# Kernel tuning notes

Hardware: AMD Instinct MI355X
Metric: run time of the kernel (lower is better)

## Reference

```python
import jax, jax.numpy as jnp
import numpy as np

B, T, C, H, K = 2, 1024, 2048, 32, 64
D_MIX, D_DEC, FF = 32, 64, 7168
GN_EPS = 1e-5 * 8 ** 2  # GroupNorm eps = 1e-5 * head_size_divisor**2


def setup_inputs() -> dict:
    key = jax.random.key(0)
    ks = jax.random.split(key, 40)
    nrm = lambda i, sh, s=0.02: jax.random.normal(ks[i], sh, jnp.float32) * s
    uni = lambda i, sh: jax.random.uniform(ks[i], sh, jnp.float32)
    return {
        'x': jax.random.normal(ks[0], (B, T, C), jnp.float32),
        'time_mix_shift': jax.random.normal(ks[1], (B, 1, C), jnp.float32),
        'channel_mix_state': jax.random.normal(ks[2], (B, 1, C), jnp.float32),
        'time_mix_state': jax.random.normal(ks[3], (B, H, K, K), jnp.float32) * 0.1,
        'ln1_w': jnp.ones((C,), jnp.float32), 'ln1_b': jnp.zeros((C,), jnp.float32),
        'ln2_w': jnp.ones((C,), jnp.float32), 'ln2_b': jnp.zeros((C,), jnp.float32),
        'maa_x': uni(4, (1, 1, C)), 'maa_w': uni(5, (1, 1, C)), 'maa_k': uni(6, (1, 1, C)),
        'maa_v': uni(7, (1, 1, C)), 'maa_r': uni(8, (1, 1, C)), 'maa_g': uni(9, (1, 1, C)),
        'maa_w1': nrm(10, (C, 5 * D_MIX), 0.01), 'maa_w2': nrm(11, (5, D_MIX, C), 0.01),
        'td': jnp.linspace(-6.0, -1.0, C, dtype=jnp.float32).reshape(1, 1, C),
        'td_w1': nrm(12, (C, D_DEC), 0.01), 'td_w2': nrm(13, (D_DEC, C), 0.01),
        'u': nrm(14, (H, K), 0.05),
        'Wr': nrm(15, (C, C)), 'Wk': nrm(16, (C, C)), 'Wv': nrm(17, (C, C)),
        'Wg': nrm(18, (C, C)), 'Wo': nrm(19, (C, C)),
        'lnx_w': jnp.ones((C,), jnp.float32), 'lnx_b': jnp.zeros((C,), jnp.float32),
        'fmaa_k': uni(20, (1, 1, C)), 'fmaa_r': uni(21, (1, 1, C)),
        'fWk': nrm(22, (FF, C)), 'fWr': nrm(23, (C, C)), 'fWv': nrm(24, (C, FF)),
    }


def _ln(x, w, b, eps=1e-5):
    m = x.mean(-1, keepdims=True)
    v = jnp.var(x, axis=-1, keepdims=True)
    return (x - m) * jax.lax.rsqrt(v + eps) * w + b


def reference(x, time_mix_shift, channel_mix_state, time_mix_state,
              ln1_w, ln1_b, ln2_w, ln2_b,
              maa_x, maa_w, maa_k, maa_v, maa_r, maa_g, maa_w1, maa_w2,
              td, td_w1, td_w2, u, Wr, Wk, Wv, Wg, Wo, lnx_w, lnx_b,
              fmaa_k, fmaa_r, fWk, fWr, fWv):
    # ---- TimeMix (att) on ln1(x) ----
    xn = _ln(x, ln1_w, ln1_b)
    prev = jnp.concatenate([time_mix_shift, xn[:, :-1]], axis=1)  # [B,T,C]
    new_shift = xn[:, -1:]
    xx = prev - xn
    hh = jnp.tanh((xn + xx * maa_x) @ maa_w1).reshape(B, T, 5, D_MIX)
    mm = jnp.einsum('btfd,fdc->fbtc', hh, maa_w2)
    xw = xn + xx * (maa_w + mm[0])
    xk = xn + xx * (maa_k + mm[1])
    xv = xn + xx * (maa_v + mm[2])
    xr = xn + xx * (maa_r + mm[3])
    xg = xn + xx * (maa_g + mm[4])
    r = xr @ Wr.T
    k = xk @ Wk.T
    v = xv @ Wv.T
    g = jax.nn.silu(xg @ Wg.T)
    # log-decay w = -exp(time_decay + LoRA(xw)); per-step decay factor is exp(w)
    w = -jnp.exp(td + jnp.tanh(xw @ td_w1) @ td_w2)
    # WKV6 recurrence over T (state [B,H,K,K])
    rs, ks_, vs, ws = (jnp.moveaxis(a.reshape(B, T, H, K), 1, 0) for a in (r, k, v, w))

    def step(s, inp):
        r_t, k_t, v_t, w_t = inp  # each [B,H,K]
        kv = jnp.einsum('bhk,bhv->bhkv', k_t, v_t)
        o_t = jnp.einsum('bhk,bhkv->bhv', r_t, s + u[None, :, :, None] * kv)
        s = jnp.exp(w_t)[..., None] * s + kv
        return s, o_t

    new_wkv, o = jax.lax.scan(step, time_mix_state, (rs, ks_, vs, ws))
    o = jnp.moveaxis(o, 0, 1)  # [B,T,H,K]
    # GroupNorm over heads (groups=H, channels=K each)
    mu = o.mean(-1, keepdims=True)
    var = jnp.var(o, axis=-1, keepdims=True)
    y = ((o - mu) * jax.lax.rsqrt(var + GN_EPS)).reshape(B, T, C) * lnx_w + lnx_b
    x = x + (y * g) @ Wo.T
    # ---- ChannelMix (ffn) on ln2(x) ----
    xn2 = _ln(x, ln2_w, ln2_b)
    prev2 = jnp.concatenate([channel_mix_state, xn2[:, :-1]], axis=1)
    new_cm = xn2[:, -1:]
    xk2 = prev2 * fmaa_k + xn2 * (1.0 - fmaa_k)
    xr2 = prev2 * fmaa_r + xn2 * (1.0 - fmaa_r)
    kv2 = (jax.nn.relu(xk2 @ fWk.T) ** 2) @ fWv.T
    x = x + jax.nn.sigmoid(xr2 @ fWr.T) * kv2
    return (x, new_shift, new_cm, new_wkv)
```

## Files before the change

### kernel.cpp

```cpp
#include <hip/hip_runtime.h>
#include <hip/hip_bf16.h>
#include <math.h>

#define BB 2
#define TT 1024
#define CC 2048
#define HH 32
#define KK 64
#define BTROWS (BB*TT)
#define FFD 7168
#define LCH 64
#define NCH (TT/LCH)

typedef unsigned short ushort_t;
typedef __bf16 bf16x8 __attribute__((ext_vector_type(8)));
typedef float f32x4 __attribute__((ext_vector_type(4)));

__device__ __forceinline__ ushort_t f2bf(float f) {
  unsigned int u = __float_as_uint(f);
  u += 0x7fff + ((u >> 16) & 1);
  return (ushort_t)(u >> 16);
}

__device__ __forceinline__ void gload16(const ushort_t* g, ushort_t* l) {
// ... 192 lines not shown
      *(float4*)&bb[4] = *(const float4*)&Bs[k][tx * 8 + 4];
#pragma unroll
      for (int i = 0; i < 8; ++i)
#pragma unroll
        for (int j = 0; j < 8; ++j) acc[i][j] = fmaf(a[i], bb[j], acc[i][j]);
    }
    __syncthreads();
  }
#pragma unroll
  for (int i = 0; i < 8; ++i) {
    int row = m0 + ty * 8 + i;
#pragma unroll
    for (int j = 0; j < 8; ++j) {
      int col = n0 + tx * 8 + j;
      out[(size_t)row * N + col] = -expf(td[col] + acc[i][j]);
    }
  }
}

struct Mix5Args {
  const float* maa[5];
  float* xw;
  ushort_t* ob[4];
};

__global__ __launch_bounds__(256) void mix5_gemm(
    const float* __restrict__ hh, const float* __restrict__ w2,
    const float* __restrict__ xn, const float* __restrict__ tms, Mix5Args args) {
  const int f = blockIdx.y;
  const int rb = blockIdx.x;
  const int tid = threadIdx.x;
  __shared__ float hh8[8][32];
  {
    int r = tid >> 5, k = tid & 31;
    hh8[r][k] = hh[(size_t)(rb * 8 + r) * 160 + f * 32 + k];
  }
  __syncthreads();
  const float* maa = args.maa[f];
  const float* w2f = w2 + (size_t)f * 32 * CC;
#pragma unroll
  for (int chunk = 0; chunk < 2; ++chunk) {
    const int col = chunk * 1024 + tid * 4;
    float4 w2v[32];
#pragma unroll
    for (int k = 0; k < 32; ++k)
      w2v[k] = *(const float4*)(w2f + (size_t)k * CC + col);
    const float4 maa4 = *(const float4*)(maa + col);
#pragma unroll
    for (int r = 0; r < 8; ++r) {
      const int row = rb * 8 + r;
      float4 acc = {0.f, 0.f, 0.f, 0.f};
#pragma unroll
      for (int k4 = 0; k4 < 8; ++k4) {
        float4 h = *(const float4*)&hh8[r][k4 * 4];
        FMA4(acc, h.x, w2v[k4 * 4 + 0]);
        FMA4(acc, h.y, w2v[k4 * 4 + 1]);
        FMA4(acc, h.z, w2v[k4 * 4 + 2]);
        FMA4(acc, h.w, w2v[k4 * 4 + 3]);
      }
      const int t = row & (TT - 1);
      const size_t oi = (size_t)row * CC + col;
      float4 xv = *(const float4*)(xn + oi);
      float4 pv;
      if (t == 0) pv = *(const float4*)(tms + (size_t)(row >> 10) * CC + col);
      else        pv = *(const float4*)(xn + oi - CC);
      float4 v;
      v.x = xv.x + (pv.x - xv.x) * (maa4.x + acc.x);
      v.y = xv.y + (pv.y - xv.y) * (maa4.y + acc.y);
      v.z = xv.z + (pv.z - xv.z) * (maa4.z + acc.z);
      v.w = xv.w + (pv.w - xv.w) * (maa4.w + acc.w);
      if (f == 0) {
        *(float4*)(args.xw + oi) = v;
      } else {
        ushort4 o;
        o.x = f2bf(v.x); o.y = f2bf(v.y); o.z = f2bf(v.z); o.w = f2bf(v.w);
        *(ushort4*)(args.ob[f - 1] + oi) = o;
      }
    }
  }
}


template <bool IS_A>
__device__ __forceinline__ void g9_stage(
    char* buf, const ushort_t* g, int ld, int r0, int k0, int tid) {
  constexpr int NJ = IS_A ? 4 : 2;
  char* dst = buf + (IS_A ? 0 : 32768);
#pragma unroll
  for (int j = 0; j < NJ; ++j) {
    int L = j * 8192 + tid * 16;
    int P = L ^ (((L >> 7) & 7) << 4);
    int r = P >> 7, cb = (P & 127) >> 1;
    gload16(g + (size_t)(r0 + r) * ld + k0 + cb, (ushort_t*)(dst + L));
  }
}

__device__ __forceinline__ void g9_core(
    const ushort_t* gA, int lda, const ushort_t* gB, int ldb,
    int m0, int n0, int kstart, int K, char* lds, f32x4 (*acc)[4]) {
  const int tid = threadIdx.x, w = tid >> 6, l = tid & 63;
  const int wr = w >> 1, wc = w & 1;
  const int r16 = l & 15, h16 = (l >> 4) * 16;
  const int NT = K >> 6;
  g9_stage<true>(lds, gA, lda, m0, kstart, tid);
  g9_stage<false>(lds, gB, ldb, n0, kstart, tid);
  g9_stage<true>(lds + 49152, gA, lda, m0, kstart + 64, tid);
  g9_stage<false>(lds + 49152, gB, ldb, n0, kstart + 64, tid);
  int cur = 0;
  for (int t = 0; t < NT; ++t) {
    char* bufc = lds + cur * 49152;
    int nxt = cur + 2; if (nxt >= 3) nxt -= 3;
    char* bufn = lds + nxt * 49152;
    if (t + 1 < NT) asm volatile("s_waitcnt vmcnt(6)" ::: "memory");
    else            asm volatile("s_waitcnt vmcnt(0)" ::: "memory");
    __builtin_amdgcn_s_barrier();
    const bool pf = (t + 2 < NT);
    const int k2 = kstart + (t + 2) * 64;
    {
      bf16x8 a[4], b[4];
#pragma unroll
      for (int mf = 0; mf < 4; ++mf) {
        int row = wr * 64 + mf * 16 + r16;
        int off = h16 ^ ((row & 7) << 4);
        a[mf] = *(const bf16x8*)(bufc + row * 128 + off);
      }
#pragma unroll
      for (int nf = 0; nf < 4; ++nf) {
        int row = wc * 64 + nf * 16 + r16;
        int off = h16 ^ ((row & 7) << 4);
        b[nf] = *(const bf16x8*)(bufc + 32768 + row * 128 + off);
      }
      if (pf) g9_stage<true>(bufn, gA, lda, m0, k2, tid);
      __builtin_amdgcn_s_setprio(1);
#pragma unroll
      for (int mf = 0; mf < 4; ++mf)
#pragma unroll
        for (int nf = 0; nf < 4; ++nf)
          acc[mf][nf] = __builtin_amdgcn_mfma_f32_16x16x32_bf16(a[mf], b[nf], acc[mf][nf], 0, 0, 0);
      __builtin_amdgcn_s_setprio(0);
    }
    {
      bf16x8 a[4], b[4];
#pragma unroll
      for (int mf = 0; mf < 4; ++mf) {
        int row = wr * 64 + mf * 16 + r16;
        int off = (64 + h16) ^ ((row & 7) << 4);
        a[mf] = *(const bf16x8*)(bufc + row * 128 + off);
      }
#pragma unroll
      for (int nf = 0; nf < 4; ++nf) {
        int row = wc * 64 + nf * 16 + r16;
        int off = (64 + h16) ^ ((row & 7) << 4);
        b[nf] = *(const bf16x8*)(bufc + 32768 + row * 128 + off);
      }
      if (pf) g9_stage<false>(bufn, gB, ldb, n0, k2, tid);
      __builtin_amdgcn_s_setprio(1);
#pragma unroll
      for (int mf = 0; mf < 4; ++mf)
#pragma unroll
        for (int nf = 0; nf < 4; ++nf)
          acc[mf][nf] = __builtin_amdgcn_mfma_f32_16x16x32_bf16(a[mf], b[nf], acc[mf][nf], 0, 0, 0);
      __builtin_amdgcn_s_setprio(0);
    }
    cur += 1; if (cur == 3) cur = 0;
  }
}

#define G9_INIT_ACC f32x4 acc[4][4]; \
  _Pragma("unroll") for (int i0 = 0; i0 < 4; ++i0) \
  _Pragma("unroll") for (int i1 = 0; i1 < 4; ++i1) acc[i0][i1] = {0.f, 0.f, 0.f, 0.f};

struct RkvgArgs {
  const ushort_t* A[4];
  const ushort_t* W[4];
  float* O[4];
};

__global__ __launch_bounds__(512, 2) void g9_rkvg(RkvgArgs args) {
  __shared__ __align__(16) char lds[147456];
  const int z = blockIdx.z;
  const int m0 = blockIdx.y * 256, n0 = blockIdx.x * 128;
  G9_INIT_ACC
  g9_core(args.A[z], CC, args.W[z], CC, m0, n0, 0, CC, lds, acc);
  const int tid = threadIdx.x, w = tid >> 6, l = tid & 63;
  const int wr = w >> 1, wc = w & 1, r16 = l & 15, q4 = (l >> 4) * 4;
  float* out = args.O[z];
  const bool silu = (z == 3);
#pragma unroll
  for (int mf = 0; mf < 4; ++mf)
#pragma unroll
    for (int nf = 0; nf < 4; ++nf) {
      int col = n0 + wc * 64 + nf * 16 + r16;
#pragma unroll
      for (int j = 0; j < 4; ++j) {
        int row = m0 + wr * 64 + mf * 16 + q4 + j;
        float v = acc[mf][nf][j];
        if (silu) v = v / (1.f + expf(-v));
        out[(size_t)row * CC + col] = v;
      }
    }
}

__global__ __launch_bounds__(512, 2) void g9_relu2(
    const ushort_t* __restrict__ A, int lda,
    const ushort_t* __restrict__ W, int ldb,
    ushort_t* __restrict__ out, int N, int K) {
  __shared__ __align__(16) char lds[147456];
  const int m0 = blockIdx.y * 256, n0 = blockIdx.x * 128;
  G9_INIT_ACC
  g9_core(A, lda, W, ldb, m0, n0, 0, K, lds, acc);
  const int tid = threadIdx.x, w = tid >> 6, l = tid & 63;
  const int wr = w >> 1, wc = w & 1, r16 = l & 15, q4 = (l >> 4) * 4;
#pragma unroll
  for (int mf = 0; mf < 4; ++mf)
#pragma unroll
    for (int nf = 0; nf < 4; ++nf) {
      int col = n0 + wc * 64 + nf * 16 + r16;
#pragma unroll
      for (int j = 0; j < 4; ++j) {
        int row = m0 + wr * 64 + mf * 16 + q4 + j;
        float r_ = fmaxf(acc[mf][nf][j], 0.f);
        out[(size_t)row * N + col] = f2bf(r_ * r_);
      }
    }
}

struct SkArgs {
  const ushort_t* A;
  const ushort_t* W;
  float* P[4];
  int lda, ldb, klen;
};

__global__ __launch_bounds__(512, 2) void g9_sk(SkArgs args) {
  __shared__ __align__(16) char lds[147456];
  const int z = blockIdx.z;
  const int m0 = blockIdx.y * 256, n0 = blockIdx.x * 128;
  G9_INIT_ACC
  g9_core(args.A, args.lda, args.W, args.ldb, m0, n0, z * args.klen, args.klen, lds, acc);
  const int tid = threadIdx.x, w = tid >> 6, l = tid & 63;
  const int wr = w >> 1, wc = w & 1, r16 = l & 15, q4 = (l >> 4) * 4;
  float* out = args.P[z];
#pragma unroll
  for (int mf = 0; mf < 4; ++mf)
#pragma unroll
    for (int nf = 0; nf < 4; ++nf) {
      int col = n0 + wc * 64 + nf * 16 + r16;
#pragma unroll
      for (int j = 0; j < 4; ++j) {
        int row = m0 + wr * 64 + mf * 16 + q4 + j;
        out[(size_t)row * CC + col] = acc[mf][nf][j];
      }
    }
}

__global__ __launch_bounds__(256) void comb_add4(
    const float* __restrict__ p0, const float* __restrict__ p1,
    const float* __restrict__ p2, const float* __restrict__ p3,
    const float* __restrict__ base, float* __restrict__ out, int n4) {
  int i = blockIdx.x * 256 + threadIdx.x;
  int stride = gridDim.x * 256;
  for (; i < n4; i += stride) {
    float4 a = ((const float4*)p0)[i];
    float4 b = ((const float4*)p1)[i];
    float4 c = ((const float4*)p2)[i];
    float4 d = ((const float4*)p3)[i];
    float4 e = ((const float4*)base)[i];
    float4 o = {e.x + a.x + b.x + c.x + d.x, e.y + a.y + b.y + c.y + d.y,
                e.z + a.z + b.z + c.z + d.z, e.w + a.w + b.w + c.w + d.w};
    ((float4*)out)[i] = o;
  }
}

__global__ __launch_bounds__(256) void comb_sig4(
    const float* __restrict__ p0, const float* __restrict__ p1,
    const float* __restrict__ p2, const float* __restrict__ p3,
    float* __restrict__ out, int n4) {
  int i = blockIdx.x * 256 + threadIdx.x;
  int stride = gridDim.x * 256;
  for (; i < n4; i += stride) {
    float4 a = ((const float4*)p0)[i];
    float4 b = ((const float4*)p1)[i];
    float4 c = ((const float4*)p2)[i];
    float4 d = ((const float4*)p3)[i];
    float4 o;
    o.x = 1.f / (1.f + expf(-(a.x + b.x + c.x + d.x)));
    o.y = 1.f / (1.f + expf(-(a.y + b.y + c.y + d.y)));
    o.z = 1.f / (1.f + expf(-(a.z + b.z + c.z + d.z)));
    o.w = 1.f / (1.f + expf(-(a.w + b.w + c.w + d.w)));
    ((float4*)out)[i] = o;
  }
}

__global__ __launch_bounds__(256) void comb_fma4(
    const float* __restrict__ p0, const float* __restrict__ p1,
    const float* __restrict__ p2, const float* __restrict__ p3,
    const float* __restrict__ x2, const float* __restrict__ sig,
    float* __restrict__ out, int n4) {
  int i = blockIdx.x * 256 + threadIdx.x;
  int stride = gridDim.x * 256;
  for (; i < n4; i += stride) {
    float4 a = ((const float4*)p0)[i];
    float4 b = ((const float4*)p1)[i];
    float4 c = ((const float4*)p2)[i];
    float4 d = ((const float4*)p3)[i];
    float4 xx = ((const float4*)x2)[i];
    float4 ss = ((const float4*)sig)[i];
    float4 o;
    o.x = fmaf(ss.x, a.x + b.x + c.x + d.x, xx.x);
    o.y = fmaf(ss.y, a.y + b.y + c.y + d.y, xx.y);
    o.z = fmaf(ss.z, a.z + b.z + c.z + d.z, xx.z);
    o.w = fmaf(ss.w, a.w + b.w + c.w + d.w, xx.w);
    ((float4*)out)[i] = o;
  }
}

__global__ __launch_bounds__(256) void wkv_chunk1(
    const float* __restrict__ r, const float* __restrict__ k,
    const float* __restrict__ v, const float* __restrict__ w,
    const float* __restrict__ u,
    float* __restrict__ rtG, float* __restrict__ Pg,
    float* __restrict__ dg, float* __restrict__ o_intra) {
  __shared__ __align__(16) float lds[4 * 4160];
  float* Ech = lds;
  float* Ach = lds;
  float* rtl = lds + 4160;
  float* ktl = lds + 2 * 4160;
  float* Vl  = lds + 3 * 4160;
  __shared__ float Dl[64], dl[64];
  const int c = blockIdx.x, bh = blockIdx.y;
  const int b = bh >> 5, h = bh & 31;
  const int tid = threadIdx.x;
  const size_t base = (size_t)b * TT * CC + (size_t)(c * LCH) * CC + h * KK;
  for (int i = 0; i < 16; ++i) {
    int e = tid + 256 * i;
    int row = e >> 6, col = e & 63;
    size_t g = base + (size_t)row * CC + col;
    rtl[row * 65 + col] = r[g];
    ktl[row * 65 + col] = k[g];
    Vl[row * 65 + col] = v[g];
  }
  if (tid < 64) {
    float cum = 0.f;
#pragma unroll 8
    for (int i = 0; i < 64; ++i) {
      cum += w[base + (size_t)i * CC + tid];
      Ech[i * 64 + tid] = cum;
    }
    float dd = expf(cum);
    dl[tid] = dd;
    dg[(size_t)(bh * NCH + c) * 64 + tid] = dd;
  }
  __syncthreads();
  {
    const int g = tid >> 6, kk = tid & 63;
    const float uk = u[h * KK + kk];
    for (int i = 0; i < 16; ++i) {
      int t = i * 4 + g;
      float Cv = Ech[t * 64 + kk];
      float Ev = (t == 0) ? 0.f : Ech[(t - 1) * 64 + kk];
      float rraw = rtl[t * 65 + kk];
      float kraw = ktl[t * 65 + kk];
      float rtv = rraw * expf(Ev);
      float ktv = kraw * expf(-Cv);
      rtl[t * 65 + kk] = rtv;
      ktl[t * 65 + kk] = ktv;
      rtG[((size_t)(bh * NCH + c) * 64 + t) * 64 + kk] = rtv;
      float prod = rraw * uk * kraw;
#pragma unroll
      for (int off = 32; off; off >>= 1) prod += __shfl_xor(prod, off);
      if (kk == 0) Dl[t] = prod;
    }
  }
  __syncthreads();
  {
    const int ti = tid >> 4, tj = tid & 15;
    float a4[4][4];
#pragma unroll
    for (int a = 0; a < 4; ++a)
#pragma unroll
      for (int q = 0; q < 4; ++q) a4[a][q] = 0.f;
    for (int kk = 0; kk < 64; ++kk) {
      float ra[4], kb[4];
#pragma unroll
      for (int a = 0; a < 4; ++a) ra[a] = rtl[(4 * ti + a) * 65 + kk];
#pragma unroll
      for (int q = 0; q < 4; ++q) kb[q] = ktl[(4 * tj + q) * 65 + kk];
#pragma unroll
      for (int a = 0; a < 4; ++a)
#pragma unroll
        for (int q = 0; q < 4; ++q) a4[a][q] = fmaf(ra[a], kb[q], a4[a][q]);
    }
#pragma unroll
    for (int a = 0; a < 4; ++a) {
      int i = 4 * ti + a;
// ... 141 lines not shown
    int row = e >> 6, col = e & 63;
    float val = (ol[row * 65 + col] - mul[row]) * rsl[row];
    val = val * lnw[h * KK + col] + lnb[h * KK + col];
    size_t gi = base + (size_t)row * CC + col;
    ym[gi] = f2bf(val * g[gi]);
  }
}

extern "C" void kernel_launch(void* const* d_in, const int* in_sizes, int n_in,
                              void* d_out, int out_size, void* d_ws, size_t ws_size,
                              hipStream_t stream) {
  const float* x    = (const float*)d_in[0];
  const float* tms  = (const float*)d_in[1];
  const float* cms  = (const float*)d_in[2];
  const float* tmstate = (const float*)d_in[3];
  const float* ln1_w = (const float*)d_in[4];
  const float* ln1_b = (const float*)d_in[5];
  const float* ln2_w = (const float*)d_in[6];
  const float* ln2_b = (const float*)d_in[7];
  const float* maa_x = (const float*)d_in[8];
  const float* maa_w = (const float*)d_in[9];
  const float* maa_k = (const float*)d_in[10];
  const float* maa_v = (const float*)d_in[11];
  const float* maa_r = (const float*)d_in[12];
  const float* maa_g = (const float*)d_in[13];
  const float* maa_w1 = (const float*)d_in[14];
  const float* maa_w2 = (const float*)d_in[15];
  const float* td    = (const float*)d_in[16];
  const float* td_w1 = (const float*)d_in[17];
  const float* td_w2 = (const float*)d_in[18];
  const float* u     = (const float*)d_in[19];
  const float* Wr    = (const float*)d_in[20];
  const float* Wk    = (const float*)d_in[21];
  const float* Wv    = (const float*)d_in[22];
  const float* Wg    = (const float*)d_in[23];
  const float* Wo    = (const float*)d_in[24];
  const float* lnx_w = (const float*)d_in[25];
  const float* lnx_b = (const float*)d_in[26];
  const float* fmk   = (const float*)d_in[27];
  const float* fmr   = (const float*)d_in[28];
  const float* fWk   = (const float*)d_in[29];
  const float* fWr   = (const float*)d_in[30];
  const float* fWv   = (const float*)d_in[31];
  (void)in_sizes; (void)n_in; (void)out_size;

  const size_t SLOT = (size_t)BTROWS * CC;
  float* F[7];
  for (int i = 0; i < 7; ++i) F[i] = (float*)d_ws + i * SLOT;
  ushort_t* B0 = (ushort_t*)((float*)d_ws + 7 * SLOT);
  ushort_t* B1 = B0 + SLOT;
  ushort_t* B2 = B1 + SLOT;
  ushort_t* B3 = B2 + SLOT;
  ushort_t* WBIG = B3 + SLOT;
  ushort_t* WrB = WBIG;
  ushort_t* WkB = WrB + (size_t)CC * CC;
  ushort_t* WvB = WkB + (size_t)CC * CC;
  ushort_t* WgB = WvB + (size_t)CC * CC;
  ushort_t* WoB = WBIG + (size_t)4 * CC * CC;
  ushort_t* fWvB = WoB + (size_t)CC * CC;
  float* hh  = (float*)(fWvB + (size_t)CC * FFD);
  float* tmpd = hh + (size_t)BTROWS * 160;
  size_t need = (size_t)((char*)(tmpd + (size_t)BTROWS * 64) - (char*)d_ws);
  if (ws_size < need) return;
  ushort_t* fWkB = WBIG;
  ushort_t* fWrB = WoB;
  ushort_t* h1   = (ushort_t*)F[5];

  float* rtG = F[1];
  float* o_intra = F[0];
  float* s_starts = (float*)B0;
  float* Pg = (float*)B2;
  float* dbuf = (float*)(WBIG + (size_t)FFD * CC);
  ushort_t* ym = B3;

  float* partsW1 = F[4];
  float* partsTD = F[5];

  float* out_x    = (float*)d_out;
  float* out_shift = out_x + (size_t)BB * TT * CC;
  float* out_cm   = out_shift + (size_t)BB * CC;
  float* out_wkv  = out_cm + (size_t)BB * CC;

  const dim3 blk256(256);
  const dim3 blk512(512);

  cvt_kernel<<<2048, blk256, 0, stream>>>(Wr, WrB, CC * CC / 4);
  cvt_kernel<<<2048, blk256, 0, stream>>>(Wk, WkB, CC * CC / 4);
  cvt_kernel<<<2048, blk256, 0, stream>>>(Wv, WvB, CC * CC / 4);
  cvt_kernel<<<2048, blk256, 0, stream>>>(Wg, WgB, CC * CC / 4);
  cvt_kernel<<<2048, blk256, 0, stream>>>(Wo, WoB, CC * CC / 4);
  cvt_kernel<<<2048, blk256, 0, stream>>>(fWv, fWvB, CC * FFD / 4);

  ln_kernel<<<BTROWS, blk256, 0, stream>>>(x, ln1_w, ln1_b, F[0], out_shift);
  mixin_kernel<<<(BTROWS * CC) / 256, blk256, 0, stream>>>(F[0], tms, maa_x, F[3]);
  gemm_splitk<<<dim3(BTROWS / 64, 3, 8), blk256, 0, stream>>>(
      F[3], CC, maa_w1, 160, partsW1, 3, CC / 8, BTROWS);
  combine_tanh<<<(BTROWS * 160 + 255) / 256, blk256, 0, stream>>>(
      partsW1, 192, BTROWS, 160, 8, hh);
  {
    Mix5Args ma;
    ma.maa[0] = maa_w; ma.maa[1] = maa_k; ma.maa[2] = maa_v; ma.maa[3] = maa_r; ma.maa[4] = maa_g;
    ma.xw = F[1];
    ma.ob[0] = B1; ma.ob[1] = B2; ma.ob[2] = B3; ma.ob[3] = B0;
    mix5_gemm<<<dim3(BTROWS / 8, 5), blk256, 0, stream>>>(hh, maa_w2, F[0], tms, ma);
  }
  gemm_splitk<<<dim3(BTROWS / 64, 1, 8), blk256, 0, stream>>>(
      F[1], CC, td_w1, 64, partsTD, 1, CC / 8, BTROWS);
  combine_tanh<<<(BTROWS * 64 + 255) / 256, blk256, 0, stream>>>(
      partsTD, 64, BTROWS, 64, 8, tmpd);
  gemm_negexp<<<dim3(16, 16), blk256, 0, stream>>>(tmpd, 64, td_w2, CC, F[2], CC, 64, td);
  {
    RkvgArgs ra;
    ra.A[0] = B3; ra.A[1] = B1; ra.A[2] = B2; ra.A[3] = B0;
    ra.W[0] = WrB; ra.W[1] = WkB; ra.W[2] = WvB; ra.W[3] = WgB;
    ra.O[0] = F[3]; ra.O[1] = F[4]; ra.O[2] = F[5]; ra.O[3] = F[6];
    g9_rkvg<<<dim3(16, 8, 4), blk512, 0, stream>>>(ra);
  }
  cvt_kernel<<<2048, blk256, 0, stream>>>(fWk, fWkB, FFD * CC / 4);
  wkv_chunk1<<<dim3(NCH, BB * HH), blk256, 0, stream>>>(
      F[3], F[4], F[5], F[2], u, rtG, Pg, dbuf, o_intra);
  wkv_chain<<<BB * HH, blk256, 0, stream>>>(Pg, dbuf, tmstate, s_starts, out_wkv);
  wkv_chunk2<<<dim3(NCH, BB * HH), blk256, 0, stream>>>(
      rtG, s_starts, o_intra, F[6], lnx_w, lnx_b, ym);
  {
    SkArgs sa;
    sa.A = ym; sa.W = WoB; sa.lda = CC; sa.ldb = CC; sa.klen = CC / 4;
    sa.P[0] = F[0]; sa.P[1] = F[1]; sa.P[2] = F[3]; sa.P[3] = F[4];
    g9_sk<<<dim3(16, 8, 4), blk512, 0, stream>>>(sa);
  }
  comb_add4<<<2048, blk256, 0, stream>>>(F[0], F[1], F[3], F[4], x, F[2], (int)(SLOT / 4));
  cvt_kernel<<<2048, blk256, 0, stream>>>(fWr, fWrB, CC * CC / 4);
  ln_kernel<<<BTROWS, blk256, 0, stream>>>(F[2], ln2_w, ln2_b, F[1], out_cm);
  mix2_kernel<<<(BTROWS * CC) / 256, blk256, 0, stream>>>(F[1], cms, fmk, fmr, B1, B2);
  g9_relu2<<<dim3(FFD / 128, 8), blk512, 0, stream>>>(B1, CC, fWkB, CC, h1, FFD, CC);
  {
    SkArgs ss;
    ss.A = B2; ss.W = fWrB; ss.lda = CC; ss.ldb = CC; ss.klen = CC / 4;
    ss.P[0] = F[0]; ss.P[1] = F[1]; ss.P[2] = F[3]; ss.P[3] = (float*)B3;
    g9_sk<<<dim3(16, 8, 4), blk512, 0, stream>>>(ss);
  }
  comb_sig4<<<2048, blk256, 0, stream>>>(F[0], F[1], F[3], (float*)B3, F[4], (int)(SLOT / 4));
  {
    SkArgs sf;
    sf.A = h1; sf.W = fWvB; sf.lda = FFD; sf.ldb = FFD; sf.klen = FFD / 4;
    sf.P[0] = F[0]; sf.P[1] = F[1]; sf.P[2] = F[3]; sf.P[3] = (float*)B0;
    g9_sk<<<dim3(16, 8, 4), blk512, 0, stream>>>(sf);
  }
  comb_fma4<<<2048, blk256, 0, stream>>>(
      F[0], F[1], F[3], (float*)B0, F[2], F[4], out_x, (int)(SLOT / 4));
}
```

Baseline: 726.0 us.

## Use 4-wave GEMM blocks with 128x64 per-wave tiles and 2-way split-K

The bf16 MFMA GEMM core now runs 256 threads per block instead of 512. The block tile stays 256x128, but each wave computes a 128x64 sub-tile (8x4 MFMA fragments), so there is more register-level reuse of LDS operands per wave. Global-to-LDS staging loads are redistributed over the smaller thread count, with the vmcnt wait adjusted to match. The split-K GEMMs (Wo, fWr, fWv) drop from 4 to 2 K-slices, which halves the partial-sum buffers read by the combine kernels. The trade-off is fewer waves per CU to hide latency, higher register pressure, and fewer blocks in the split-K launches.

After: 866.0 us. 19.3% more time.

```diff
diff --git a/kernel.cpp b/kernel.cpp
--- a/kernel.cpp
+++ b/kernel.cpp
@@ -298,45 +298,45 @@
 
 
 template <bool IS_A>
-__device__ __forceinline__ void g9_stage(
+__device__ __forceinline__ void g10_stage(
     char* buf, const ushort_t* g, int ld, int r0, int k0, int tid) {
-  constexpr int NJ = IS_A ? 4 : 2;
+  constexpr int NJ = IS_A ? 8 : 4;
   char* dst = buf + (IS_A ? 0 : 32768);
 #pragma unroll
   for (int j = 0; j < NJ; ++j) {
-    int L = j * 8192 + tid * 16;
+    int L = j * 4096 + tid * 16;
     int P = L ^ (((L >> 7) & 7) << 4);
     int r = P >> 7, cb = (P & 127) >> 1;
     gload16(g + (size_t)(r0 + r) * ld + k0 + cb, (ushort_t*)(dst + L));
   }
 }
 
-__device__ __forceinline__ void g9_core(
+__device__ __forceinline__ void g10_core(
     const ushort_t* gA, int lda, const ushort_t* gB, int ldb,
     int m0, int n0, int kstart, int K, char* lds, f32x4 (*acc)[4]) {
   const int tid = threadIdx.x, w = tid >> 6, l = tid & 63;
   const int wr = w >> 1, wc = w & 1;
   const int r16 = l & 15, h16 = (l >> 4) * 16;
   const int NT = K >> 6;
-  g9_stage<true>(lds, gA, lda, m0, kstart, tid);
-  g9_stage<false>(lds, gB, ldb, n0, kstart, tid);
-  g9_stage<true>(lds + 49152, gA, lda, m0, kstart + 64, tid);
-  g9_stage<false>(lds + 49152, gB, ldb, n0, kstart + 64, tid);
+  g10_stage<true>(lds, gA, lda, m0, kstart, tid);
+  g10_stage<false>(lds, gB, ldb, n0, kstart, tid);
+  g10_stage<true>(lds + 49152, gA, lda, m0, kstart + 64, tid);
+  g10_stage<false>(lds + 49152, gB, ldb, n0, kstart + 64, tid);
   int cur = 0;
   for (int t = 0; t < NT; ++t) {
     char* bufc = lds + cur * 49152;
     int nxt = cur + 2; if (nxt >= 3) nxt -= 3;
     char* bufn = lds + nxt * 49152;
-    if (t + 1 < NT) asm volatile("s_waitcnt vmcnt(6)" ::: "memory");
+    if (t + 1 < NT) asm volatile("s_waitcnt vmcnt(12)" ::: "memory");
     else            asm volatile("s_waitcnt vmcnt(0)" ::: "memory");
     __builtin_amdgcn_s_barrier();
     const bool pf = (t + 2 < NT);
     const int k2 = kstart + (t + 2) * 64;
     {
-      bf16x8 a[4], b[4];
-#pragma unroll
-      for (int mf = 0; mf < 4; ++mf) {
-        int row = wr * 64 + mf * 16 + r16;
+      bf16x8 a[8], b[4];
+#pragma unroll
+      for (int mf = 0; mf < 8; ++mf) {
+        int row = wr * 128 + mf * 16 + r16;
         int off = h16 ^ ((row & 7) << 4);
         a[mf] = *(const bf16x8*)(bufc + row * 128 + off);
       }
@@ -346,20 +346,20 @@
         int off = h16 ^ ((row & 7) << 4);
         b[nf] = *(const bf16x8*)(bufc + 32768 + row * 128 + off);
       }
-      if (pf) g9_stage<true>(bufn, gA, lda, m0, k2, tid);
+      if (pf) g10_stage<true>(bufn, gA, lda, m0, k2, tid);
       __builtin_amdgcn_s_setprio(1);
 #pragma unroll
-      for (int mf = 0; mf < 4; ++mf)
+      for (int mf = 0; mf < 8; ++mf)
 #pragma unroll
         for (int nf = 0; nf < 4; ++nf)
           acc[mf][nf] = __builtin_amdgcn_mfma_f32_16x16x32_bf16(a[mf], b[nf], acc[mf][nf], 0, 0, 0);
       __builtin_amdgcn_s_setprio(0);
     }
     {
-      bf16x8 a[4], b[4];
-#pragma unroll
-      for (int mf = 0; mf < 4; ++mf) {
-        int row = wr * 64 + mf * 16 + r16;
+      bf16x8 a[8], b[4];
+#pragma unroll
+      for (int mf = 0; mf < 8; ++mf) {
+        int row = wr * 128 + mf * 16 + r16;
         int off = (64 + h16) ^ ((row & 7) << 4);
         a[mf] = *(const bf16x8*)(bufc + row * 128 + off);
       }
@@ -369,10 +369,10 @@
         int off = (64 + h16) ^ ((row & 7) << 4);
         b[nf] = *(const bf16x8*)(bufc + 32768 + row * 128 + off);
       }
-      if (pf) g9_stage<false>(bufn, gB, ldb, n0, k2, tid);
+      if (pf) g10_stage<false>(bufn, gB, ldb, n0, k2, tid);
       __builtin_amdgcn_s_setprio(1);
 #pragma unroll
-      for (int mf = 0; mf < 4; ++mf)
+      for (int mf = 0; mf < 8; ++mf)
 #pragma unroll
         for (int nf = 0; nf < 4; ++nf)
           acc[mf][nf] = __builtin_amdgcn_mfma_f32_16x16x32_bf16(a[mf], b[nf], acc[mf][nf], 0, 0, 0);
@@ -382,8 +382,8 @@
   }
 }
 
-#define G9_INIT_ACC f32x4 acc[4][4]; \
-  _Pragma("unroll") for (int i0 = 0; i0 < 4; ++i0) \
+#define G10_INIT_ACC f32x4 acc[8][4]; \
+  _Pragma("unroll") for (int i0 = 0; i0 < 8; ++i0) \
   _Pragma("unroll") for (int i1 = 0; i1 < 4; ++i1) acc[i0][i1] = {0.f, 0.f, 0.f, 0.f};
 
 struct RkvgArgs {
@@ -392,24 +392,24 @@
   float* O[4];
 };
 
-__global__ __launch_bounds__(512, 2) void g9_rkvg(RkvgArgs args) {
+__global__ __launch_bounds__(256) void g10_rkvg(RkvgArgs args) {
   __shared__ __align__(16) char lds[147456];
   const int z = blockIdx.z;
   const int m0 = blockIdx.y * 256, n0 = blockIdx.x * 128;
-  G9_INIT_ACC
-  g9_core(args.A[z], CC, args.W[z], CC, m0, n0, 0, CC, lds, acc);
+  G10_INIT_ACC
+  g10_core(args.A[z], CC, args.W[z], CC, m0, n0, 0, CC, lds, acc);
   const int tid = threadIdx.x, w = tid >> 6, l = tid & 63;
   const int wr = w >> 1, wc = w & 1, r16 = l & 15, q4 = (l >> 4) * 4;
   float* out = args.O[z];
   const bool silu = (z == 3);
 #pragma unroll
-  for (int mf = 0; mf < 4; ++mf)
+  for (int mf = 0; mf < 8; ++mf)
 #pragma unroll
     for (int nf = 0; nf < 4; ++nf) {
       int col = n0 + wc * 64 + nf * 16 + r16;
 #pragma unroll
       for (int j = 0; j < 4; ++j) {
-        int row = m0 + wr * 64 + mf * 16 + q4 + j;
+        int row = m0 + wr * 128 + mf * 16 + q4 + j;
         float v = acc[mf][nf][j];
         if (silu) v = v / (1.f + expf(-v));
         out[(size_t)row * CC + col] = v;
@@ -417,24 +417,24 @@
     }
 }
 
-__global__ __launch_bounds__(512, 2) void g9_relu2(
+__global__ __launch_bounds__(256) void g10_relu2(
     const ushort_t* __restrict__ A, int lda,
     const ushort_t* __restrict__ W, int ldb,
     ushort_t* __restrict__ out, int N, int K) {
   __shared__ __align__(16) char lds[147456];
   const int m0 = blockIdx.y * 256, n0 = blockIdx.x * 128;
-  G9_INIT_ACC
-  g9_core(A, lda, W, ldb, m0, n0, 0, K, lds, acc);
+  G10_INIT_ACC
+  g10_core(A, lda, W, ldb, m0, n0, 0, K, lds, acc);
   const int tid = threadIdx.x, w = tid >> 6, l = tid & 63;
   const int wr = w >> 1, wc = w & 1, r16 = l & 15, q4 = (l >> 4) * 4;
 #pragma unroll
-  for (int mf = 0; mf < 4; ++mf)
+  for (int mf = 0; mf < 8; ++mf)
 #pragma unroll
     for (int nf = 0; nf < 4; ++nf) {
       int col = n0 + wc * 64 + nf * 16 + r16;
 #pragma unroll
       for (int j = 0; j < 4; ++j) {
-        int row = m0 + wr * 64 + mf * 16 + q4 + j;
+        int row = m0 + wr * 128 + mf * 16 + q4 + j;
         float r_ = fmaxf(acc[mf][nf][j], 0.f);
         out[(size_t)row * N + col] = f2bf(r_ * r_);
       }
@@ -444,73 +444,65 @@
 struct SkArgs {
   const ushort_t* A;
   const ushort_t* W;
-  float* P[4];
+  float* P[2];
   int lda, ldb, klen;
 };
 
-__global__ __launch_bounds__(512, 2) void g9_sk(SkArgs args) {
+__global__ __launch_bounds__(256) void g10_sk(SkArgs args) {
   __shared__ __align__(16) char lds[147456];
   const int z = blockIdx.z;
   const int m0 = blockIdx.y * 256, n0 = blockIdx.x * 128;
-  G9_INIT_ACC
-  g9_core(args.A, args.lda, args.W, args.ldb, m0, n0, z * args.klen, args.klen, lds, acc);
+  G10_INIT_ACC
+  g10_core(args.A, args.lda, args.W, args.ldb, m0, n0, z * args.klen, args.klen, lds, acc);
   const int tid = threadIdx.x, w = tid >> 6, l = tid & 63;
   const int wr = w >> 1, wc = w & 1, r16 = l & 15, q4 = (l >> 4) * 4;
   float* out = args.P[z];
 #pragma unroll
-  for (int mf = 0; mf < 4; ++mf)
+  for (int mf = 0; mf < 8; ++mf)
 #pragma unroll
     for (int nf = 0; nf < 4; ++nf) {
       int col = n0 + wc * 64 + nf * 16 + r16;
 #pragma unroll
       for (int j = 0; j < 4; ++j) {
-        int row = m0 + wr * 64 + mf * 16 + q4 + j;
+        int row = m0 + wr * 128 + mf * 16 + q4 + j;
         out[(size_t)row * CC + col] = acc[mf][nf][j];
       }
     }
 }
 
-__global__ __launch_bounds__(256) void comb_add4(
+__global__ __launch_bounds__(256) void comb_add2(
     const float* __restrict__ p0, const float* __restrict__ p1,
-    const float* __restrict__ p2, const float* __restrict__ p3,
     const float* __restrict__ base, float* __restrict__ out, int n4) {
   int i = blockIdx.x * 256 + threadIdx.x;
   int stride = gridDim.x * 256;
   for (; i < n4; i += stride) {
     float4 a = ((const float4*)p0)[i];
     float4 b = ((const float4*)p1)[i];
-    float4 c = ((const float4*)p2)[i];
-    float4 d = ((const float4*)p3)[i];
-    float4 e = ((const float4*)base)[i];
-    float4 o = {e.x + a.x + b.x + c.x + d.x, e.y + a.y + b.y + c.y + d.y,
-                e.z + a.z + b.z + c.z + d.z, e.w + a.w + b.w + c.w + d.w};
+    float4 c = ((const float4*)base)[i];
+    float4 o = {c.x + a.x + b.x, c.y + a.y + b.y, c.z + a.z + b.z, c.w + a.w + b.w};
     ((float4*)out)[i] = o;
   }
 }
 
-__global__ __launch_bounds__(256) void comb_sig4(
+__global__ __launch_bounds__(256) void comb_sig2(
     const float* __restrict__ p0, const float* __restrict__ p1,
-    const float* __restrict__ p2, const float* __restrict__ p3,
     float* __restrict__ out, int n4) {
   int i = blockIdx.x * 256 + threadIdx.x;
   int stride = gridDim.x * 256;
   for (; i < n4; i += stride) {
     float4 a = ((const float4*)p0)[i];
     float4 b = ((const float4*)p1)[i];
-    float4 c = ((const float4*)p2)[i];
-    float4 d = ((const float4*)p3)[i];
     float4 o;
-    o.x = 1.f / (1.f + expf(-(a.x + b.x + c.x + d.x)));
-    o.y = 1.f / (1.f + expf(-(a.y + b.y + c.y + d.y)));
-    o.z = 1.f / (1.f + expf(-(a.z + b.z + c.z + d.z)));
-    o.w = 1.f / (1.f + expf(-(a.w + b.w + c.w + d.w)));
+    o.x = 1.f / (1.f + expf(-(a.x + b.x)));
+    o.y = 1.f / (1.f + expf(-(a.y + b.y)));
+    o.z = 1.f / (1.f + expf(-(a.z + b.z)));
+    o.w = 1.f / (1.f + expf(-(a.w + b.w)));
     ((float4*)out)[i] = o;
   }
 }
 
-__global__ __launch_bounds__(256) void comb_fma4(
+__global__ __launch_bounds__(256) void comb_fma2(
     const float* __restrict__ p0, const float* __restrict__ p1,
-    const float* __restrict__ p2, const float* __restrict__ p3,
     const float* __restrict__ x2, const float* __restrict__ sig,
     float* __restrict__ out, int n4) {
   int i = blockIdx.x * 256 + threadIdx.x;
@@ -518,15 +510,13 @@
   for (; i < n4; i += stride) {
     float4 a = ((const float4*)p0)[i];
     float4 b = ((const float4*)p1)[i];
-    float4 c = ((const float4*)p2)[i];
-    float4 d = ((const float4*)p3)[i];
     float4 xx = ((const float4*)x2)[i];
     float4 ss = ((const float4*)sig)[i];
     float4 o;
-    o.x = fmaf(ss.x, a.x + b.x + c.x + d.x, xx.x);
-    o.y = fmaf(ss.y, a.y + b.y + c.y + d.y, xx.y);
-    o.z = fmaf(ss.z, a.z + b.z + c.z + d.z, xx.z);
-    o.w = fmaf(ss.w, a.w + b.w + c.w + d.w, xx.w);
+    o.x = fmaf(ss.x, a.x + b.x, xx.x);
+    o.y = fmaf(ss.y, a.y + b.y, xx.y);
+    o.z = fmaf(ss.z, a.z + b.z, xx.z);
+    o.w = fmaf(ss.w, a.w + b.w, xx.w);
     ((float4*)out)[i] = o;
   }
 }
@@ -834,7 +824,6 @@
   float* out_wkv  = out_cm + (size_t)BB * CC;
 
   const dim3 blk256(256);
-  const dim3 blk512(512);
 
   cvt_kernel<<<2048, blk256, 0, stream>>>(Wr, WrB, CC * CC / 4);
   cvt_kernel<<<2048, blk256, 0, stream>>>(Wk, WkB, CC * CC / 4);
@@ -866,7 +855,7 @@
     ra.A[0] = B3; ra.A[1] = B1; ra.A[2] = B2; ra.A[3] = B0;
     ra.W[0] = WrB; ra.W[1] = WkB; ra.W[2] = WvB; ra.W[3] = WgB;
     ra.O[0] = F[3]; ra.O[1] = F[4]; ra.O[2] = F[5]; ra.O[3] = F[6];
-    g9_rkvg<<<dim3(16, 8, 4), blk512, 0, stream>>>(ra);
+    g10_rkvg<<<dim3(16, 8, 4), blk256, 0, stream>>>(ra);
   }
   cvt_kernel<<<2048, blk256, 0, stream>>>(fWk, fWkB, FFD * CC / 4);
   wkv_chunk1<<<dim3(NCH, BB * HH), blk256, 0, stream>>>(
@@ -876,28 +865,28 @@
       rtG, s_starts, o_intra, F[6], lnx_w, lnx_b, ym);
   {
     SkArgs sa;
-    sa.A = ym; sa.W = WoB; sa.lda = CC; sa.ldb = CC; sa.klen = CC / 4;
-    sa.P[0] = F[0]; sa.P[1] = F[1]; sa.P[2] = F[3]; sa.P[3] = F[4];
-    g9_sk<<<dim3(16, 8, 4), blk512, 0, stream>>>(sa);
-  }
-  comb_add4<<<2048, blk256, 0, stream>>>(F[0], F[1], F[3], F[4], x, F[2], (int)(SLOT / 4));
+    sa.A = ym; sa.W = WoB; sa.lda = CC; sa.ldb = CC; sa.klen = CC / 2;
+    sa.P[0] = F[0]; sa.P[1] = F[1];
+    g10_sk<<<dim3(16, 8, 2), blk256, 0, stream>>>(sa);
+  }
+  comb_add2<<<2048, blk256, 0, stream>>>(F[0], F[1], x, F[2], (int)(SLOT / 4));
   cvt_kernel<<<2048, blk256, 0, stream>>>(fWr, fWrB, CC * CC / 4);
   ln_kernel<<<BTROWS, blk256, 0, stream>>>(F[2], ln2_w, ln2_b, F[1], out_cm);
   mix2_kernel<<<(BTROWS * CC) / 256, blk256, 0, stream>>>(F[1], cms, fmk, fmr, B1, B2);
-  g9_relu2<<<dim3(FFD / 128, 8), blk512, 0, stream>>>(B1, CC, fWkB, CC, h1, FFD, CC);
+  g10_relu2<<<dim3(FFD / 128, 8), blk256, 0, stream>>>(B1, CC, fWkB, CC, h1, FFD, CC);
   {
     SkArgs ss;
-    ss.A = B2; ss.W = fWrB; ss.lda = CC; ss.ldb = CC; ss.klen = CC / 4;
-    ss.P[0] = F[0]; ss.P[1] = F[1]; ss.P[2] = F[3]; ss.P[3] = (float*)B3;
-    g9_sk<<<dim3(16, 8, 4), blk512, 0, stream>>>(ss);
-  }
-  comb_sig4<<<2048, blk256, 0, stream>>>(F[0], F[1], F[3], (float*)B3, F[4], (int)(SLOT / 4));
+    ss.A = B2; ss.W = fWrB; ss.lda = CC; ss.ldb = CC; ss.klen = CC / 2;
+    ss.P[0] = F[0]; ss.P[1] = F[3];
+    g10_sk<<<dim3(16, 8, 2), blk256, 0, stream>>>(ss);
+  }
+  comb_sig2<<<2048, blk256, 0, stream>>>(F[0], F[3], F[4], (int)(SLOT / 4));
   {
     SkArgs sf;
-    sf.A = h1; sf.W = fWvB; sf.lda = FFD; sf.ldb = FFD; sf.klen = FFD / 4;
-    sf.P[0] = F[0]; sf.P[1] = F[1]; sf.P[2] = F[3]; sf.P[3] = (float*)B0;
-    g9_sk<<<dim3(16, 8, 4), blk512, 0, stream>>>(sf);
-  }
-  comb_fma4<<<2048, blk256, 0, stream>>>(
-      F[0], F[1], F[3], (float*)B0, F[2], F[4], out_x, (int)(SLOT / 4));
-}
+    sf.A = h1; sf.W = fWvB; sf.lda = FFD; sf.ldb = FFD; sf.klen = FFD / 2;
+    sf.P[0] = F[0]; sf.P[1] = F[3];
+    g10_sk<<<dim3(16, 8, 2), blk256, 0, stream>>>(sf);
+  }
+  comb_fma2<<<2048, blk256, 0, stream>>>(
+      F[0], F[3], F[2], F[4], out_x, (int)(SLOT / 4));
+}
```

## Use 4-wave GEMM blocks with 128x64 warp tiles and BK=32 stages

Applied to the files above, without the earlier changes.

The bf16 MFMA GEMM core drops from 8 waves per block to 4, so each wave computes a 128x64 tile (8x4 MFMA fragments) instead of 64x64. The K step per stage halves to 32 with a matching 4-way LDS swizzle, which halves LDS use to 72KB. The aim is more MFMA work per LDS fragment load and more resident blocks per CU. In exchange each wave holds twice the accumulator registers, which may lower occupancy, and each stage has more barriers relative to its compute.

Result: slower. 855.3 us (+17.8%).

```diff
diff --git a/kernel.cpp b/kernel.cpp
--- a/kernel.cpp
+++ b/kernel.cpp
@@ -298,92 +298,70 @@
 
 
 template <bool IS_A>
-__device__ __forceinline__ void g9_stage(
+__device__ __forceinline__ void g11_stage(
     char* buf, const ushort_t* g, int ld, int r0, int k0, int tid) {
   constexpr int NJ = IS_A ? 4 : 2;
-  char* dst = buf + (IS_A ? 0 : 32768);
+  char* dst = buf + (IS_A ? 0 : 16384);
 #pragma unroll
   for (int j = 0; j < NJ; ++j) {
-    int L = j * 8192 + tid * 16;
-    int P = L ^ (((L >> 7) & 7) << 4);
-    int r = P >> 7, cb = (P & 127) >> 1;
+    int L = j * 4096 + tid * 16;
+    int P = L ^ (((L >> 7) & 3) << 4);
+    int r = P >> 6, cb = (P & 63) >> 1;
     gload16(g + (size_t)(r0 + r) * ld + k0 + cb, (ushort_t*)(dst + L));
   }
 }
 
-__device__ __forceinline__ void g9_core(
+__device__ __forceinline__ void g11_core(
     const ushort_t* gA, int lda, const ushort_t* gB, int ldb,
     int m0, int n0, int kstart, int K, char* lds, f32x4 (*acc)[4]) {
   const int tid = threadIdx.x, w = tid >> 6, l = tid & 63;
   const int wr = w >> 1, wc = w & 1;
-  const int r16 = l & 15, h16 = (l >> 4) * 16;
-  const int NT = K >> 6;
-  g9_stage<true>(lds, gA, lda, m0, kstart, tid);
-  g9_stage<false>(lds, gB, ldb, n0, kstart, tid);
-  g9_stage<true>(lds + 49152, gA, lda, m0, kstart + 64, tid);
-  g9_stage<false>(lds + 49152, gB, ldb, n0, kstart + 64, tid);
+  const int r16 = l & 15, h16b = (l >> 4) * 16;
+  const int NT = K >> 5;
+  g11_stage<true>(lds, gA, lda, m0, kstart, tid);
+  g11_stage<false>(lds, gB, ldb, n0, kstart, tid);
+  g11_stage<true>(lds + 24576, gA, lda, m0, kstart + 32, tid);
+  g11_stage<false>(lds + 24576, gB, ldb, n0, kstart + 32, tid);
   int cur = 0;
   for (int t = 0; t < NT; ++t) {
-    char* bufc = lds + cur * 49152;
+    char* bufc = lds + cur * 24576;
     int nxt = cur + 2; if (nxt >= 3) nxt -= 3;
-    char* bufn = lds + nxt * 49152;
+    char* bufn = lds + nxt * 24576;
     if (t + 1 < NT) asm volatile("s_waitcnt vmcnt(6)" ::: "memory");
     else            asm volatile("s_waitcnt vmcnt(0)" ::: "memory");
     __builtin_amdgcn_s_barrier();
     const bool pf = (t + 2 < NT);
-    const int k2 = kstart + (t + 2) * 64;
-    {
-      bf16x8 a[4], b[4];
-#pragma unroll
-      for (int mf = 0; mf < 4; ++mf) {
-        int row = wr * 64 + mf * 16 + r16;
-        int off = h16 ^ ((row & 7) << 4);
-        a[mf] = *(const bf16x8*)(bufc + row * 128 + off);
-      }
-#pragma unroll
-      for (int nf = 0; nf < 4; ++nf) {
-        int row = wc * 64 + nf * 16 + r16;
-        int off = h16 ^ ((row & 7) << 4);
-        b[nf] = *(const bf16x8*)(bufc + 32768 + row * 128 + off);
-      }
-      if (pf) g9_stage<true>(bufn, gA, lda, m0, k2, tid);
-      __builtin_amdgcn_s_setprio(1);
-#pragma unroll
-      for (int mf = 0; mf < 4; ++mf)
-#pragma unroll
-        for (int nf = 0; nf < 4; ++nf)
-          acc[mf][nf] = __builtin_amdgcn_mfma_f32_16x16x32_bf16(a[mf], b[nf], acc[mf][nf], 0, 0, 0);
-      __builtin_amdgcn_s_setprio(0);
-    }
-    {
-      bf16x8 a[4], b[4];
-#pragma unroll
-      for (int mf = 0; mf < 4; ++mf) {
-        int row = wr * 64 + mf * 16 + r16;
-        int off = (64 + h16) ^ ((row & 7) << 4);
-        a[mf] = *(const bf16x8*)(bufc + row * 128 + off);
-      }
-#pragma unroll
-      for (int nf = 0; nf < 4; ++nf) {
-        int row = wc * 64 + nf * 16 + r16;
-        int off = (64 + h16) ^ ((row & 7) << 4);
-        b[nf] = *(const bf16x8*)(bufc + 32768 + row * 128 + off);
-      }
-      if (pf) g9_stage<false>(bufn, gB, ldb, n0, k2, tid);
-      __builtin_amdgcn_s_setprio(1);
-#pragma unroll
-      for (int mf = 0; mf < 4; ++mf)
-#pragma unroll
-        for (int nf = 0; nf < 4; ++nf)
-          acc[mf][nf] = __builtin_amdgcn_mfma_f32_16x16x32_bf16(a[mf], b[nf], acc[mf][nf], 0, 0, 0);
-      __builtin_amdgcn_s_setprio(0);
-    }
+    const int k2 = kstart + (t + 2) * 32;
+    bf16x8 a[8], b[4];
+#pragma unroll
+    for (int mf = 0; mf < 8; ++mf) {
+      int row = wr * 128 + mf * 16 + r16;
+      int off = h16b ^ (((row >> 1) & 3) << 4);
+      a[mf] = *(const bf16x8*)(bufc + row * 64 + off);
+    }
+#pragma unroll
+    for (int nf = 0; nf < 4; ++nf) {
+      int row = wc * 64 + nf * 16 + r16;
+      int off = h16b ^ (((row >> 1) & 3) << 4);
+      b[nf] = *(const bf16x8*)(bufc + 16384 + row * 64 + off);
+    }
+    if (pf) {
+      g11_stage<true>(bufn, gA, lda, m0, k2, tid);
+      g11_stage<false>(bufn, gB, ldb, n0, k2, tid);
+    }
+    __builtin_amdgcn_s_setprio(1);
+#pragma unroll
+    for (int mf = 0; mf < 8; ++mf)
+#pragma unroll
+      for (int nf = 0; nf < 4; ++nf)
+        acc[mf][nf] = __builtin_amdgcn_mfma_f32_16x16x32_bf16(a[mf], b[nf], acc[mf][nf], 0, 0, 0);
+    __builtin_amdgcn_s_setprio(0);
     cur += 1; if (cur == 3) cur = 0;
   }
 }
 
-#define G9_INIT_ACC f32x4 acc[4][4]; \
-  _Pragma("unroll") for (int i0 = 0; i0 < 4; ++i0) \
+#define G11_INIT_ACC f32x4 acc[8][4]; \
+  _Pragma("unroll") for (int i0 = 0; i0 < 8; ++i0) \
   _Pragma("unroll") for (int i1 = 0; i1 < 4; ++i1) acc[i0][i1] = {0.f, 0.f, 0.f, 0.f};
 
 struct RkvgArgs {
@@ -392,24 +370,24 @@
   float* O[4];
 };
 
-__global__ __launch_bounds__(512, 2) void g9_rkvg(RkvgArgs args) {
-  __shared__ __align__(16) char lds[147456];
+__global__ __launch_bounds__(256) void g11_rkvg(RkvgArgs args) {
+  __shared__ __align__(16) char lds[73728];
   const int z = blockIdx.z;
   const int m0 = blockIdx.y * 256, n0 = blockIdx.x * 128;
-  G9_INIT_ACC
-  g9_core(args.A[z], CC, args.W[z], CC, m0, n0, 0, CC, lds, acc);
+  G11_INIT_ACC
+  g11_core(args.A[z], CC, args.W[z], CC, m0, n0, 0, CC, lds, acc);
   const int tid = threadIdx.x, w = tid >> 6, l = tid & 63;
   const int wr = w >> 1, wc = w & 1, r16 = l & 15, q4 = (l >> 4) * 4;
   float* out = args.O[z];
   const bool silu = (z == 3);
 #pragma unroll
-  for (int mf = 0; mf < 4; ++mf)
+  for (int mf = 0; mf < 8; ++mf)
 #pragma unroll
     for (int nf = 0; nf < 4; ++nf) {
       int col = n0 + wc * 64 + nf * 16 + r16;
 #pragma unroll
       for (int j = 0; j < 4; ++j) {
-        int row = m0 + wr * 64 + mf * 16 + q4 + j;
+        int row = m0 + wr * 128 + mf * 16 + q4 + j;
         float v = acc[mf][nf][j];
         if (silu) v = v / (1.f + expf(-v));
         out[(size_t)row * CC + col] = v;
@@ -417,24 +395,24 @@
     }
 }
 
-__global__ __launch_bounds__(512, 2) void g9_relu2(
+__global__ __launch_bounds__(256) void g11_relu2(
     const ushort_t* __restrict__ A, int lda,
     const ushort_t* __restrict__ W, int ldb,
     ushort_t* __restrict__ out, int N, int K) {
-  __shared__ __align__(16) char lds[147456];
+  __shared__ __align__(16) char lds[73728];
   const int m0 = blockIdx.y * 256, n0 = blockIdx.x * 128;
-  G9_INIT_ACC
-  g9_core(A, lda, W, ldb, m0, n0, 0, K, lds, acc);
+  G11_INIT_ACC
+  g11_core(A, lda, W, ldb, m0, n0, 0, K, lds, acc);
   const int tid = threadIdx.x, w = tid >> 6, l = tid & 63;
   const int wr = w >> 1, wc = w & 1, r16 = l & 15, q4 = (l >> 4) * 4;
 #pragma unroll
-  for (int mf = 0; mf < 4; ++mf)
+  for (int mf = 0; mf < 8; ++mf)
 #pragma unroll
     for (int nf = 0; nf < 4; ++nf) {
       int col = n0 + wc * 64 + nf * 16 + r16;
 #pragma unroll
       for (int j = 0; j < 4; ++j) {
-        int row = m0 + wr * 64 + mf * 16 + q4 + j;
+        int row = m0 + wr * 128 + mf * 16 + q4 + j;
         float r_ = fmaxf(acc[mf][nf][j], 0.f);
         out[(size_t)row * N + col] = f2bf(r_ * r_);
       }
@@ -448,23 +426,23 @@
   int lda, ldb, klen;
 };
 
-__global__ __launch_bounds__(512, 2) void g9_sk(SkArgs args) {
-  __shared__ __align__(16) char lds[147456];
+__global__ __launch_bounds__(256) void g11_sk(SkArgs args) {
+  __shared__ __align__(16) char lds[73728];
   const int z = blockIdx.z;
   const int m0 = blockIdx.y * 256, n0 = blockIdx.x * 128;
-  G9_INIT_ACC
-  g9_core(args.A, args.lda, args.W, args.ldb, m0, n0, z * args.klen, args.klen, lds, acc);
+  G11_INIT_ACC
+  g11_core(args.A, args.lda, args.W, args.ldb, m0, n0, z * args.klen, args.klen, lds, acc);
   const int tid = threadIdx.x, w = tid >> 6, l = tid & 63;
   const int wr = w >> 1, wc = w & 1, r16 = l & 15, q4 = (l >> 4) * 4;
   float* out = args.P[z];
 #pragma unroll
-  for (int mf = 0; mf < 4; ++mf)
+  for (int mf = 0; mf < 8; ++mf)
 #pragma unroll
     for (int nf = 0; nf < 4; ++nf) {
       int col = n0 + wc * 64 + nf * 16 + r16;
 #pragma unroll
       for (int j = 0; j < 4; ++j) {
-        int row = m0 + wr * 64 + mf * 16 + q4 + j;
+        int row = m0 + wr * 128 + mf * 16 + q4 + j;
         out[(size_t)row * CC + col] = acc[mf][nf][j];
       }
     }
@@ -834,7 +812,6 @@
   float* out_wkv  = out_cm + (size_t)BB * CC;
 
   const dim3 blk256(256);
-  const dim3 blk512(512);
 
   cvt_kernel<<<2048, blk256, 0, stream>>>(Wr, WrB, CC * CC / 4);
   cvt_kernel<<<2048, blk256, 0, stream>>>(Wk, WkB, CC * CC / 4);
@@ -866,7 +843,7 @@
     ra.A[0] = B3; ra.A[1] = B1; ra.A[2] = B2; ra.A[3] = B0;
     ra.W[0] = WrB; ra.W[1] = WkB; ra.W[2] = WvB; ra.W[3] = WgB;
     ra.O[0] = F[3]; ra.O[1] = F[4]; ra.O[2] = F[5]; ra.O[3] = F[6];
-    g9_rkvg<<<dim3(16, 8, 4), blk512, 0, stream>>>(ra);
+    g11_rkvg<<<dim3(16, 8, 4), blk256, 0, stream>>>(ra);
   }
   cvt_kernel<<<2048, blk256, 0, stream>>>(fWk, fWkB, FFD * CC / 4);
   wkv_chunk1<<<dim3(NCH, BB * HH), blk256, 0, stream>>>(
@@ -878,25 +855,25 @@
     SkArgs sa;
     sa.A = ym; sa.W = WoB; sa.lda = CC; sa.ldb = CC; sa.klen = CC / 4;
     sa.P[0] = F[0]; sa.P[1] = F[1]; sa.P[2] = F[3]; sa.P[3] = F[4];
-    g9_sk<<<dim3(16, 8, 4), blk512, 0, stream>>>(sa);
+    g11_sk<<<dim3(16, 8, 4), blk256, 0, stream>>>(sa);
   }
   comb_add4<<<2048, blk256, 0, stream>>>(F[0], F[1], F[3], F[4], x, F[2], (int)(SLOT / 4));
   cvt_kernel<<<2048, blk256, 0, stream>>>(fWr, fWrB, CC * CC / 4);
   ln_kernel<<<BTROWS, blk256, 0, stream>>>(F[2], ln2_w, ln2_b, F[1], out_cm);
   mix2_kernel<<<(BTROWS * CC) / 256, blk256, 0, stream>>>(F[1], cms, fmk, fmr, B1, B2);
-  g9_relu2<<<dim3(FFD / 128, 8), blk512, 0, stream>>>(B1, CC, fWkB, CC, h1, FFD, CC);
+  g11_relu2<<<dim3(FFD / 128, 8), blk256, 0, stream>>>(B1, CC, fWkB, CC, h1, FFD, CC);
   {
     SkArgs ss;
     ss.A = B2; ss.W = fWrB; ss.lda = CC; ss.ldb = CC; ss.klen = CC / 4;
     ss.P[0] = F[0]; ss.P[1] = F[1]; ss.P[2] = F[3]; ss.P[3] = (float*)B3;
-    g9_sk<<<dim3(16, 8, 4), blk512, 0, stream>>>(ss);
+    g11_sk<<<dim3(16, 8, 4), blk256, 0, stream>>>(ss);
   }
   comb_sig4<<<2048, blk256, 0, stream>>>(F[0], F[1], F[3], (float*)B3, F[4], (int)(SLOT / 4));
   {
     SkArgs sf;
     sf.A = h1; sf.W = fWvB; sf.lda = FFD; sf.ldb = FFD; sf.klen = FFD / 4;
     sf.P[0] = F[0]; sf.P[1] = F[1]; sf.P[2] = F[3]; sf.P[3] = (float*)B0;
-    g9_sk<<<dim3(16, 8, 4), blk512, 0, stream>>>(sf);
+    g11_sk<<<dim3(16, 8, 4), blk256, 0, stream>>>(sf);
   }
   comb_fma4<<<2048, blk256, 0, stream>>>(
       F[0], F[1], F[3], (float*)B0, F[2], F[4], out_x, (int)(SLOT / 4));
```
